# Performance work log

Measured on AMD Instinct MI355X. Metric: run time of the kernel, lower is better.

Reference implementation:

```python
import jax, jax.numpy as jnp
import numpy as np

D_MODEL = 1024
HEADS = 16
D_K = D_MODEL // HEADS
B, S = 2, 2048


def setup_inputs() -> dict:
    key = jax.random.key(0)
    ks = jax.random.split(key, 11)
    sc = 1.0 / np.sqrt(D_MODEL)
    inp = {
        "q": jax.random.normal(ks[0], (B, S, D_MODEL), jnp.float32),
        "k": jax.random.normal(ks[1], (B, S, D_MODEL), jnp.float32),
        "v": jax.random.normal(ks[2], (B, S, D_MODEL), jnp.float32),
        # causal mask, broadcastable to (B, H, S, S); 0 -> masked
        "mask": jnp.tril(jnp.ones((S, S), jnp.int32))[None, None],
        "w_q": jax.random.normal(ks[3], (D_MODEL, D_MODEL), jnp.float32) * sc,
        "b_q": jax.random.normal(ks[4], (D_MODEL,), jnp.float32) * sc,
        "w_k": jax.random.normal(ks[5], (D_MODEL, D_MODEL), jnp.float32) * sc,
        "b_k": jax.random.normal(ks[6], (D_MODEL,), jnp.float32) * sc,
        "w_v": jax.random.normal(ks[7], (D_MODEL, D_MODEL), jnp.float32) * sc,
        "b_v": jax.random.normal(ks[8], (D_MODEL,), jnp.float32) * sc,
        "w_o": jax.random.normal(ks[9], (D_MODEL, D_MODEL), jnp.float32) * sc,
        "b_o": jax.random.normal(ks[10], (D_MODEL,), jnp.float32) * sc,
    }
    return inp


def reference(q, k, v, mask, w_q, b_q, w_k, b_k, w_v, b_v, w_o, b_o):
    b = q.shape[0]
    # torch Linear: x @ W.T + b
    Q = q @ w_q.T + b_q
    K = k @ w_k.T + b_k
    V = v @ w_v.T + b_v
    # (B, S, D) -> (B, H, S, d_k)
    Q = Q.reshape(b, -1, HEADS, D_K).transpose(0, 2, 1, 3)
    K = K.reshape(b, -1, HEADS, D_K).transpose(0, 2, 1, 3)
    V = V.reshape(b, -1, HEADS, D_K).transpose(0, 2, 1, 3)
    scores = jnp.einsum("bhqd,bhkd->bhqk", Q, K) / np.sqrt(D_K).astype(np.float32)
    scores = jnp.where(mask == 0, -jnp.inf, scores)
    attn = jax.nn.softmax(scores, axis=-1)
    out = jnp.einsum("bhqk,bhkd->bhqd", attn, V)
    out = out.transpose(0, 2, 1, 3).reshape(b, -1, D_MODEL)
    # dropout is identity in eval mode
    return out @ w_o.T + b_o
```

## Files before the change

### kernel.cpp

```cpp
#include <hip/hip_runtime.h>
#include <math.h>

#define D_MODEL 1024
#define N_HEADS 16
#define DKH     64
#define BATCH   2
#define SEQ     2048
#define NT      (SEQ/64)

typedef unsigned short u16;
typedef __attribute__((ext_vector_type(8))) short short8;
typedef __attribute__((ext_vector_type(4))) float f32x4;

__device__ __forceinline__ u16 f2bf(float f) {
    unsigned u = __float_as_uint(f);
    u += 0x7fffu + ((u >> 16) & 1u);
    return (u16)(u >> 16);
}

__device__ __forceinline__ void gll16(const void* g, void* l) {
    __builtin_amdgcn_global_load_lds((const __attribute__((address_space(1))) void*)g,
                                     (__attribute__((address_space(3))) void*)l, 16, 0, 0);
}

__global__ __launch_bounds__(256)
void convert_kernel(const float* __restrict__ q, const float* __restrict__ k,
                    const float* __restrict__ v, const float* __restrict__ wq,
                    const float* __restrict__ wk, const float* __restrict__ wv,
                    const float* __restrict__ wo,
                    u16* __restrict__ qb, u16* __restrict__ kb, u16* __restrict__ vb,
                    u16* __restrict__ wqb, u16* __restrict__ wkb,
                    u16* __restrict__ wvb, u16* __restrict__ wob)
{
    const size_t NV = ((size_t)16 << 20) >> 3;
    for (size_t i = (size_t)blockIdx.x * blockDim.x + threadIdx.x; i < NV;
         i += (size_t)gridDim.x * blockDim.x) {
        const size_t e = i << 3;
        const float* s; u16* d; size_t off;
        if (e < ((size_t)12 << 20)) {
            const int seg = (int)(e >> 22);
            off = e & (((size_t)1 << 22) - 1);
            s = seg == 0 ? q : seg == 1 ? k : v;
            d = seg == 0 ? qb : seg == 1 ? kb : vb;
        } else {
            const size_t r = e - ((size_t)12 << 20);
            const int seg = (int)(r >> 20);
            off = r & (((size_t)1 << 20) - 1);
            s = seg == 0 ? wq : seg == 1 ? wk : seg == 2 ? wv : wo;
            d = seg == 0 ? wqb : seg == 1 ? wkb : seg == 2 ? wvb : wob;
        }
        const float4 f0 = *(const float4*)(s + off);
        const float4 f1 = *(const float4*)(s + off + 4);
        short8 o;
        o[0]=(short)f2bf(f0.x); o[1]=(short)f2bf(f0.y); o[2]=(short)f2bf(f0.z); o[3]=(short)f2bf(f0.w);
        o[4]=(short)f2bf(f1.x); o[5]=(short)f2bf(f1.y); o[6]=(short)f2bf(f1.z); o[7]=(short)f2bf(f1.w);
        *(short8*)(d + off) = o;
    }
}

#define GEMM_PREAMBLE                                                            \
    __shared__ __align__(16) u16 As[2][128][32];                                 \
    __shared__ __align__(16) u16 Bs[2][128][32];                                 \
    const int tid  = threadIdx.x;                                                \
    const int lane = tid & 63;                                                   \
    const int wid  = tid >> 6;                                                   \
    const int wm   = wid >> 1, wn = wid & 1;                                     \
    const int lr   = lane & 15, lg = lane >> 4;                                  \
    const int mb   = blockIdx.x * 128, nb = blockIdx.y * 128;                    \
    const int g_row = lane >> 2;                                                 \
    const int g_col = (lane & 3) << 3;                                           \
    const u16* Ab = A  + (size_t)mb * K;                                         \
    const u16* Bb = Bw + (size_t)nb * K;                                         \
    f32x4 acc[4][4];                                                             \
    _Pragma("unroll")                                                            \
    for (int i = 0; i < 4; ++i)                                                  \
        _Pragma("unroll")                                                        \
        for (int j = 0; j < 4; ++j) { f32x4 z = {0.f,0.f,0.f,0.f}; acc[i][j] = z; }

#define STAGE(buf, kt)                                                           \
    {                                                                            \
        _Pragma("unroll")                                                        \
        for (int t = 0; t < 2; ++t) {                                            \
            const int r0 = t*64 + wid*16;                                        \
            gll16(&Ab[(size_t)(r0 + g_row)*K + (kt) + g_col], &As[buf][r0][0]);  \
            gll16(&Bb[(size_t)(r0 + g_row)*K + (kt) + g_col], &Bs[buf][r0][0]);  \
        }                                                                        \
    }

#define GEMM_MAINLOOP                                                            \
    STAGE(0, 0)                                                                  \
    __syncthreads();                                                             \
    const int NK = K >> 5;                                                       \
    for (int it = 0; it < NK; ++it) {                                            \
        const int c = it & 1;                                                    \
        if (it + 1 < NK) STAGE(c ^ 1, (it + 1) << 5)                             \
        short8 a[4], b[4];                                                       \
        _Pragma("unroll")                                                        \
        for (int i = 0; i < 4; ++i) a[i] = *(const short8*)&As[c][wm*64 + i*16 + lr][lg*8]; \
        _Pragma("unroll")                                                        \
        for (int j = 0; j < 4; ++j) b[j] = *(const short8*)&Bs[c][wn*64 + j*16 + lr][lg*8]; \
        _Pragma("unroll")                                                        \
        for (int i = 0; i < 4; ++i)                                              \
            _Pragma("unroll")                                                    \
            for (int j = 0; j < 4; ++j)                                          \
                acc[i][j] = __builtin_amdgcn_mfma_f32_16x16x32_bf16(a[i], b[j], acc[i][j], 0, 0, 0); \
        __syncthreads();                                                         \
    }

__global__ __launch_bounds__(256, 3)
void gemm_qkv_kernel(const u16* __restrict__ qb, const u16* __restrict__ kb,
                     const u16* __restrict__ vb, const u16* __restrict__ wqb,
                     const u16* __restrict__ wkb, const u16* __restrict__ wvb,
                     const float* __restrict__ b_q, const float* __restrict__ b_k,
                     const float* __restrict__ b_v,
                     u16* __restrict__ Qh, u16* __restrict__ Kh, u16* __restrict__ Vt,
                     int M, int N, int K)
{
    const int z = blockIdx.z;
    const u16* A    = z == 0 ? qb  : z == 1 ? kb  : vb;
    const u16* Bw   = z == 0 ? wqb : z == 1 ? wkb : wvb;
    const float* bias = z == 0 ? b_q : z == 1 ? b_k : b_v;
    u16* dst        = z == 0 ? Qh  : z == 1 ? Kh  : Vt;
    const float scale = z == 0 ? 0.125f : 1.0f;

    GEMM_PREAMBLE
    GEMM_MAINLOOP

    #pragma unroll
    for (int i = 0; i < 4; ++i) {
        #pragma unroll
        for (int j = 0; j < 4; ++j) {
            const int mbase = mb + wm*64 + i*16 + lg*4;
            const int n     = nb + wn*64 + j*16 + lr;
            const float bn  = bias[n];
            const int h = n >> 6, d = n & 63;
            #pragma unroll
            for (int r = 0; r < 4; ++r) {
                const int m = mbase + r;
                const int b = m >> 11, s = m & (SEQ - 1);
                const float val = (acc[i][j][r] + bn) * scale;
                if (z == 2)
                    dst[(((size_t)(b*N_HEADS + h))*DKH + d)*SEQ + s] = f2bf(val);
                else
                    dst[(((size_t)(b*N_HEADS + h))*SEQ + s)*DKH + d] = f2bf(val);
            }
        }
    }
}

__global__ __launch_bounds__(256)
void gemm_out_kernel(const u16* __restrict__ A, const u16* __restrict__ Bw,
                     const float* __restrict__ bias, float* __restrict__ dst,
                     int M, int N, int K)
{
    GEMM_PREAMBLE
    GEMM_MAINLOOP

    #pragma unroll
    for (int i = 0; i < 4; ++i) {
        #pragma unroll
        for (int j = 0; j < 4; ++j) {
            const int mbase = mb + wm*64 + i*16 + lg*4;
            const int n     = nb + wn*64 + j*16 + lr;
            const float bn  = bias[n];
            #pragma unroll
            for (int r = 0; r < 4; ++r)
                dst[(size_t)(mbase + r) * N + n] = acc[i][j][r] + bn;
        }
    }
}

__device__ __forceinline__ void attn_step(
    const short8& aq0, const short8& aq1,
    f32x4 (&o)[4], f32x4& osum, float (&m_run)[4],
    const u16 (*__restrict__ Kl)[64], const u16 (*__restrict__ Vl)[64],
    u16 (*__restrict__ Pw)[72],
    int kvb, int qbw, int lr, int lg)
{
    const int ksw = (lr & 7) << 3;
    f32x4 s[4];
    #pragma unroll
    for (int cb = 0; cb < 4; ++cb) {
        const int kr = cb*16 + lr;
        f32x4 z = {0.f,0.f,0.f,0.f};
        short8 k0 = *(const short8*)&Kl[kr][( 0 + lg*8) ^ ksw];
        short8 k1 = *(const short8*)&Kl[kr][(32 + lg*8) ^ ksw];
        z = __builtin_amdgcn_mfma_f32_16x16x32_bf16(aq0, k0, z, 0, 0, 0);
        z = __builtin_amdgcn_mfma_f32_16x16x32_bf16(aq1, k1, z, 0, 0, 0);
        s[cb] = z;
    }

    if (kvb + 63 > qbw) {
        #pragma unroll
        for (int cb = 0; cb < 4; ++cb)
            #pragma unroll
            for (int r = 0; r < 4; ++r)
                if (kvb + cb*16 + lr > qbw + lg*4 + r) s[cb][r] = -INFINITY;
    }

    float tm[4];
    #pragma unroll
    for (int r = 0; r < 4; ++r) {
        float t = fmaxf(fmaxf(s[0][r], s[1][r]), fmaxf(s[2][r], s[3][r]));
        #pragma unroll
        for (int off = 1; off < 16; off <<= 1) t = fmaxf(t, __shfl_xor(t, off));
        tm[r] = t;
    }
    int need = 0;
    #pragma unroll
    for (int r = 0; r < 4; ++r) need |= (tm[r] > m_run[r] + 8.f) ? 1 : 0;
    if (__any(need)) {
        #pragma unroll
        for (int r = 0; r < 4; ++r) {
            const float mnew  = fmaxf(m_run[r], tm[r]);
            const float alpha = __expf(m_run[r] - mnew);
            m_run[r] = mnew;
            osum[r] *= alpha;
            #pragma unroll
            for (int db = 0; db < 4; ++db) o[db][r] *= alpha;
        }
    }
    #pragma unroll
    for (int r = 0; r < 4; ++r)
        #pragma unroll
        for (int cb = 0; cb < 4; ++cb)
            Pw[lg*4 + r][cb*16 + lr] = f2bf(__expf(s[cb][r] - m_run[r]));

    short8 vone;
    #pragma unroll
    for (int j = 0; j < 8; ++j) vone[j] = (short)0x3F80;
    #pragma unroll
    for (int ks = 0; ks < 2; ++ks) {
        short8 ap = *(short8*)&Pw[lr][ks*32 + lg*8];
        #pragma unroll
        for (int db = 0; db < 4; ++db) {
            const int vr = db*16 + lr;
            short8 bv = *(const short8*)&Vl[vr][(ks*32 + lg*8) ^ ksw];
            o[db] = __builtin_amdgcn_mfma_f32_16x16x32_bf16(ap, bv, o[db], 0, 0, 0);
        }
        osum = __builtin_amdgcn_mfma_f32_16x16x32_bf16(ap, vone, osum, 0, 0, 0);
    }
}

__global__ __launch_bounds__(512, 4)
void flash_attn_kernel(const u16* __restrict__ Qh, const u16* __restrict__ Kh,
                       const u16* __restrict__ Vt, u16* __restrict__ attb)
{
    __shared__ __align__(16) u16 Kl[2][64][64];
    __shared__ __align__(16) u16 Vl[2][64][64];
    __shared__ __align__(16) u16 P[8][16][72];

    const int tid  = threadIdx.x;
    const int lane = tid & 63;
    const int wid  = tid >> 6;
    const int lr   = lane & 15, lg = lane >> 4;
    const int bh   = blockIdx.x;
    const int t    = 15 - blockIdx.y;
    const int qbw  = t*128 + wid*16;
    const size_t base = (size_t)bh * SEQ * DKH;

    const int srow = tid >> 3;
    const int se0  = (tid & 7) << 3;
    const int sec  = se0 ^ ((srow & 7) << 3);

    short8 aq0 = *(const short8*)&Qh[base + (size_t)(qbw + lr)*DKH +  0 + lg*8];
    short8 aq1 = *(const short8*)&Qh[base + (size_t)(qbw + lr)*DKH + 32 + lg*8];

    f32x4 o[4], osum;
    float m_run[4];
    #pragma unroll
    for (int r = 0; r < 4; ++r) m_run[r] = -INFINITY;
    {
        f32x4 z = {0.f,0.f,0.f,0.f};
        osum = z;
        #pragma unroll
        for (int db = 0; db < 4; ++db) o[db] = z;
    }

    const int nc = 2 * (t + 1);

    {
        short8 k0 = *(const short8*)&Kh[base + (size_t)srow*DKH + se0];
        short8 v0 = *(const short8*)&Vt[base + (size_t)srow*SEQ + se0];
        *(short8*)&Kl[0][srow][sec] = k0;
        *(short8*)&Vl[0][srow][sec] = v0;
    }
    __syncthreads();

    int cur = 0;
    for (int c = 0; c < nc; ++c) {
        const int kvb = c * 64;
        short8 nk0, nv0;
        const bool pref = (c + 1 < nc);
        if (pref) {
            const int nb_ = kvb + 64;
            nk0 = *(const short8*)&Kh[base + (size_t)(nb_ + srow)*DKH + se0];
            nv0 = *(const short8*)&Vt[base + (size_t)srow*SEQ + nb_ + se0];
        }

        if (kvb <= qbw + 15)
            attn_step(aq0, aq1, o, osum, m_run, Kl[cur], Vl[cur], P[wid], kvb, qbw, lr, lg);

        __syncthreads();
        if (pref) {
            *(short8*)&Kl[cur^1][srow][sec] = nk0;
            *(short8*)&Vl[cur^1][srow][sec] = nv0;
        }
        __syncthreads();
        cur ^= 1;
    }

    const int b = bh >> 4, h = bh & 15;
    float inv[4];
    #pragma unroll
    for (int r = 0; r < 4; ++r) inv[r] = 1.f / osum[r];
    #pragma unroll
    for (int db = 0; db < 4; ++db) {
        #pragma unroll
        for (int r = 0; r < 4; ++r) {
            const int s_ = qbw + lg*4 + r;
            attb[((size_t)(b*SEQ + s_))*D_MODEL + h*64 + db*16 + lr] = f2bf(o[db][r] * inv[r]);
        }
    }
}

extern "C" void kernel_launch(void* const* d_in, const int* in_sizes, int n_in,
                              void* d_out, int out_size, void* d_ws, size_t ws_size,
                              hipStream_t stream)
{
    const float* q   = (const float*)d_in[0];
    const float* k   = (const float*)d_in[1];
    const float* v   = (const float*)d_in[2];
    const float* w_q = (const float*)d_in[4];
    const float* b_q = (const float*)d_in[5];
    const float* w_k = (const float*)d_in[6];
    const float* b_k = (const float*)d_in[7];
    const float* w_v = (const float*)d_in[8];
    const float* b_v = (const float*)d_in[9];
    const float* w_o = (const float*)d_in[10];
    const float* b_o = (const float*)d_in[11];

    char* ws = (char*)d_ws;
    const size_t MB = 1024*1024;
    u16* Qh   = (u16*)(ws +  0*MB);
    u16* Kh   = (u16*)(ws +  8*MB);
    u16* Vt   = (u16*)(ws + 16*MB);
    u16* qb   = (u16*)(ws + 24*MB);
    u16* kb   = (u16*)(ws + 32*MB);
    u16* vb   = (u16*)(ws + 40*MB);
    u16* wqb  = (u16*)(ws + 48*MB);
    u16* wkb  = (u16*)(ws + 50*MB);
    u16* wvb  = (u16*)(ws + 52*MB);
    u16* wob  = (u16*)(ws + 54*MB);
    u16* attb = qb;

    const int M = BATCH * SEQ, N = D_MODEL, K = D_MODEL;

    convert_kernel<<<2048, 256, 0, stream>>>(q, k, v, w_q, w_k, w_v, w_o,
                                             qb, kb, vb, wqb, wkb, wvb, wob);
    gemm_qkv_kernel<<<dim3(M/128, N/128, 3), 256, 0, stream>>>(
        qb, kb, vb, wqb, wkb, wvb, b_q, b_k, b_v, Qh, Kh, Vt, M, N, K);
    flash_attn_kernel<<<dim3(BATCH*N_HEADS, 16), 512, 0, stream>>>(Qh, Kh, Vt, attb);
    gemm_out_kernel<<<dim3(M/128, N/128), 256, 0, stream>>>(attb, wob, b_o, (float*)d_out, M, N, K);
}
```

Before: 141.2 us.

## Split causal flash attention along KV into chunks and merge partials

Causal attention is split along the KV axis into chunks of up to 8 KV tiles. Each query tile gets 1-4 blocks, so the work per block is balanced and the grid grows from 512 to 1280 blocks. Each block writes unnormalised bf16 partial outputs plus its running max and sum. A new merge kernel combines them with log-sum-exp rescaling. The row-max reduction also switches from shuffles to DPP row_ror. The cost is an extra kernel launch, extra partial-result traffic, bf16 rounding of the partials, and workspace reuse for the partial buffers.

```diff
diff --git a/kernel.cpp b/kernel.cpp
--- a/kernel.cpp
+++ b/kernel.cpp
@@ -6,7 +6,8 @@
 #define DKH     64
 #define BATCH   2
 #define SEQ     2048
-#define NT      (SEQ/64)
+#define NT128   (SEQ/128)
+#define PARTS_PER_BH 40
 
 typedef unsigned short u16;
 typedef __attribute__((ext_vector_type(8))) short short8;
@@ -17,10 +18,27 @@
     u += 0x7fffu + ((u >> 16) & 1u);
     return (u16)(u >> 16);
 }
+__device__ __forceinline__ float bf2f(u16 x) {
+    return __int_as_float(((int)x) << 16);
+}
 
 __device__ __forceinline__ void gll16(const void* g, void* l) {
     __builtin_amdgcn_global_load_lds((const __attribute__((address_space(1))) void*)g,
                                      (__attribute__((address_space(3))) void*)l, 16, 0, 0);
+}
+
+template<int CTRL>
+__device__ __forceinline__ float rormax(float x) {
+    int r = __builtin_amdgcn_update_dpp(__float_as_int(x), __float_as_int(x),
+                                        CTRL, 0xf, 0xf, false);
+    return fmaxf(x, __int_as_float(r));
+}
+__device__ __forceinline__ float rowmax16(float x) {
+    x = rormax<0x121>(x);
+    x = rormax<0x122>(x);
+    x = rormax<0x124>(x);
+    x = rormax<0x128>(x);
+    return x;
 }
 
 __global__ __launch_bounds__(256)
@@ -200,12 +218,9 @@
 
     float tm[4];
     #pragma unroll
-    for (int r = 0; r < 4; ++r) {
-        float t = fmaxf(fmaxf(s[0][r], s[1][r]), fmaxf(s[2][r], s[3][r]));
-        #pragma unroll
-        for (int off = 1; off < 16; off <<= 1) t = fmaxf(t, __shfl_xor(t, off));
-        tm[r] = t;
-    }
+    for (int r = 0; r < 4; ++r)
+        tm[r] = rowmax16(fmaxf(fmaxf(s[0][r], s[1][r]), fmaxf(s[2][r], s[3][r])));
+
     int need = 0;
     #pragma unroll
     for (int r = 0; r < 4; ++r) need |= (tm[r] > m_run[r] + 8.f) ? 1 : 0;
@@ -242,22 +257,32 @@
     }
 }
 
-__global__ __launch_bounds__(512, 4)
-void flash_attn_kernel(const u16* __restrict__ Qh, const u16* __restrict__ Kh,
-                       const u16* __restrict__ Vt, u16* __restrict__ attb)
+__global__ __launch_bounds__(512)
+void flash_split_kernel(const u16* __restrict__ Qh, const u16* __restrict__ Kh,
+                        const u16* __restrict__ Vt, u16* __restrict__ part_o,
+                        float* __restrict__ part_ms)
 {
     __shared__ __align__(16) u16 Kl[2][64][64];
     __shared__ __align__(16) u16 Vl[2][64][64];
     __shared__ __align__(16) u16 P[8][16][72];
+
+    const int x = blockIdx.x;
+    int t, ch;
+    if      (x <  4) { t = x;                 ch = 0;        }
+    else if (x < 12) { t = 4 + ((x-4) >> 1);  ch = (x-4)&1;  }
+    else if (x < 24) { t = 8 + (x-12)/3;      ch = (x-12)%3; }
+    else             { t = 12 + ((x-24) >> 2); ch = (x-24)&3; }
 
     const int tid  = threadIdx.x;
     const int lane = tid & 63;
     const int wid  = tid >> 6;
     const int lr   = lane & 15, lg = lane >> 4;
-    const int bh   = blockIdx.x;
-    const int t    = 15 - blockIdx.y;
+    const int bh   = blockIdx.y;
     const int qbw  = t*128 + wid*16;
     const size_t base = (size_t)bh * SEQ * DKH;
+
+    const int c0      = ch * 8;
+    const int nc_here = min(8, 2*(t+1) - c0);
 
     const int srow = tid >> 3;
     const int se0  = (tid & 7) << 3;
@@ -277,21 +302,20 @@
         for (int db = 0; db < 4; ++db) o[db] = z;
     }
 
-    const int nc = 2 * (t + 1);
-
     {
-        short8 k0 = *(const short8*)&Kh[base + (size_t)srow*DKH + se0];
-        short8 v0 = *(const short8*)&Vt[base + (size_t)srow*SEQ + se0];
+        const int kb0 = c0 * 64;
+        short8 k0 = *(const short8*)&Kh[base + (size_t)(kb0 + srow)*DKH + se0];
+        short8 v0 = *(const short8*)&Vt[base + (size_t)srow*SEQ + kb0 + se0];
         *(short8*)&Kl[0][srow][sec] = k0;
         *(short8*)&Vl[0][srow][sec] = v0;
     }
     __syncthreads();
 
     int cur = 0;
-    for (int c = 0; c < nc; ++c) {
-        const int kvb = c * 64;
+    for (int ci = 0; ci < nc_here; ++ci) {
+        const int kvb = (c0 + ci) * 64;
         short8 nk0, nv0;
-        const bool pref = (c + 1 < nc);
+        const bool pref = (ci + 1 < nc_here);
         if (pref) {
             const int nb_ = kvb + 64;
             nk0 = *(const short8*)&Kh[base + (size_t)(nb_ + srow)*DKH + se0];
@@ -310,17 +334,70 @@
         cur ^= 1;
     }
 
+    const size_t slot = (size_t)bh * PARTS_PER_BH + x;
+    u16*   po = part_o  + (slot << 13);
+    float* pm = part_ms + (slot << 8);
+    #pragma unroll
+    for (int db = 0; db < 4; ++db)
+        #pragma unroll
+        for (int r = 0; r < 4; ++r)
+            po[(wid*16 + lg*4 + r)*64 + db*16 + lr] = f2bf(o[db][r]);
+    if (lr == 0) {
+        #pragma unroll
+        for (int r = 0; r < 4; ++r) {
+            pm[(wid*16 + lg*4 + r)*2 + 0] = m_run[r];
+            pm[(wid*16 + lg*4 + r)*2 + 1] = osum[r];
+        }
+    }
+}
+
+__global__ __launch_bounds__(256)
+void merge_kernel(const u16* __restrict__ part_o, const float* __restrict__ part_ms,
+                  u16* __restrict__ attb)
+{
+    const int t   = blockIdx.x;
+    const int bh  = blockIdx.y;
+    const int nch = min(4, (2*(t+1) + 7) >> 3);
+    const int basex = t < 4 ? t : t < 8 ? 4 + 2*(t-4) : t < 12 ? 12 + 3*(t-8) : 24 + 4*(t-12);
+
+    const int row = threadIdx.x >> 1;
+    const int cb  = (threadIdx.x & 1) * 32;
+
+    float mm[4], ss[4];
+    float M = -INFINITY;
+    for (int c = 0; c < nch; ++c) {
+        const size_t slot = (size_t)bh * PARTS_PER_BH + basex + c;
+        mm[c] = part_ms[(slot << 8) + row*2 + 0];
+        ss[c] = part_ms[(slot << 8) + row*2 + 1];
+        M = fmaxf(M, mm[c]);
+    }
+    float S = 0.f;
+    float acc[32];
+    #pragma unroll
+    for (int j = 0; j < 32; ++j) acc[j] = 0.f;
+    for (int c = 0; c < nch; ++c) {
+        const float w = __expf(mm[c] - M);
+        S += w * ss[c];
+        const size_t slot = (size_t)bh * PARTS_PER_BH + basex + c;
+        const u16* po = part_o + (slot << 13) + row*64 + cb;
+        #pragma unroll
+        for (int g = 0; g < 4; ++g) {
+            short8 v = *(const short8*)(po + g*8);
+            #pragma unroll
+            for (int j = 0; j < 8; ++j)
+                acc[g*8 + j] += w * bf2f((u16)v[j]);
+        }
+    }
+    const float inv = 1.f / S;
     const int b = bh >> 4, h = bh & 15;
-    float inv[4];
-    #pragma unroll
-    for (int r = 0; r < 4; ++r) inv[r] = 1.f / osum[r];
-    #pragma unroll
-    for (int db = 0; db < 4; ++db) {
-        #pragma unroll
-        for (int r = 0; r < 4; ++r) {
-            const int s_ = qbw + lg*4 + r;
-            attb[((size_t)(b*SEQ + s_))*D_MODEL + h*64 + db*16 + lr] = f2bf(o[db][r] * inv[r]);
-        }
+    const int grow = t*128 + row;
+    u16* dst = attb + ((size_t)(b*SEQ + grow))*D_MODEL + h*64 + cb;
+    #pragma unroll
+    for (int g = 0; g < 4; ++g) {
+        short8 ov;
+        #pragma unroll
+        for (int j = 0; j < 8; ++j) ov[j] = (short)f2bf(acc[g*8 + j] * inv);
+        *(short8*)(dst + g*8) = ov;
     }
 }
 
@@ -353,6 +430,8 @@
     u16* wvb  = (u16*)(ws + 52*MB);
     u16* wob  = (u16*)(ws + 54*MB);
     u16* attb = qb;
+    u16*   part_o  = (u16*)(ws + 32*MB);
+    float* part_ms = (float*)(ws + 52*MB);
 
     const int M = BATCH * SEQ, N = D_MODEL, K = D_MODEL;
 
@@ -360,6 +439,8 @@
                                              qb, kb, vb, wqb, wkb, wvb, wob);
     gemm_qkv_kernel<<<dim3(M/128, N/128, 3), 256, 0, stream>>>(
         qb, kb, vb, wqb, wkb, wvb, b_q, b_k, b_v, Qh, Kh, Vt, M, N, K);
-    flash_attn_kernel<<<dim3(BATCH*N_HEADS, 16), 512, 0, stream>>>(Qh, Kh, Vt, attb);
+    flash_split_kernel<<<dim3(PARTS_PER_BH, BATCH*N_HEADS), 512, 0, stream>>>(
+        Qh, Kh, Vt, part_o, part_ms);
+    merge_kernel<<<dim3(NT128, BATCH*N_HEADS), 256, 0, stream>>>(part_o, part_ms, attb);
     gemm_out_kernel<<<dim3(M/128, N/128), 256, 0, stream>>>(attb, wob, b_o, (float*)d_out, M, N, K);
 }
```

New measurement: 143.6 us. About the same (+1.7%).
